# Performance work log

Hardware: AMD Instinct MI355X
Metric: run time of the kernel (lower is better)

## Reference

```python
import jax, jax.numpy as jnp
import numpy as np

B, H, W, C = 8, 64, 64, 512
C8, C2 = C // 8, C // 2  # f/g channels = 64, h channels = 256 (divisor = 2)


def _maxpool2x2(t):
    # [B, H, W, F] -> [B, H//2, W//2, F], valid 2x2 max pooling
    b, h, w, f = t.shape
    return t.reshape(b, h // 2, 2, w // 2, 2, f).max(axis=(2, 4))


def setup_inputs() -> dict:
    key = jax.random.key(0)
    kx, kf, kg, kh, ko, kgam = jax.random.split(key, 6)
    sf = lambda fan_in: (1.0 / np.sqrt(fan_in)).astype(np.float32)
    return {
        "x": jax.random.normal(kx, (B, H, W, C), dtype=jnp.float32),
        "wf": jax.random.normal(kf, (C, C8), dtype=jnp.float32) * sf(C),
        "wg": jax.random.normal(kg, (C, C8), dtype=jnp.float32) * sf(C),
        "wh": jax.random.normal(kh, (C, C2), dtype=jnp.float32) * sf(C),
        "wo": jax.random.normal(ko, (C2, C), dtype=jnp.float32) * sf(C2),
        "gamma": jax.random.normal(kgam, (1,), dtype=jnp.float32) * 0.1,
    }


def reference(x, wf, wg, wh, wo, gamma):
    b = x.shape[0]
    # 1x1 convs == channel matmuls
    f = _maxpool2x2(jnp.einsum("bhwc,cd->bhwd", x, wf)).reshape(b, -1, C8)  # [B, N/4, C/8]
    g = jnp.einsum("bhwc,cd->bhwd", x, wg).reshape(b, -1, C8)               # [B, N,   C/8]
    s = jnp.einsum("bqd,bkd->bqk", g, f)                                     # unscaled scores
    beta = jax.nn.softmax(s, axis=-1)
    h = _maxpool2x2(jnp.einsum("bhwc,cd->bhwd", x, wh)).reshape(b, -1, C2)  # [B, N/4, C/2]
    o = jnp.einsum("bqk,bkd->bqd", beta, h).reshape(b, H, W, C2)
    o = jnp.einsum("bhwd,dc->bhwc", o, wo)                                   # o_conv back to C
    return gamma * o + x
```

## Files before the change

### kernel.cpp

```cpp
#include <hip/hip_runtime.h>
#include <hip/hip_bf16.h>

#define NTOK 4096
#define NPOOL 1024

using short8 = __attribute__((ext_vector_type(8))) short;
using f32x4  = __attribute__((ext_vector_type(4))) float;

__device__ __forceinline__ unsigned short f2bf(float f) {
  __hip_bfloat16 h = __float2bfloat16(f);
  return __builtin_bit_cast(unsigned short, h);
}

__device__ __forceinline__ int pool_row(int bx, int m) {
  int pg = bx * 16 + (m >> 2);
  int corner = m & 3;
  int batch = pg >> 10;
  int pl = pg & 1023;
  int pi = pl >> 5, pj = pl & 31;
  return (batch << 12) + ((2 * pi + (corner >> 1)) << 6) + 2 * pj + (corner & 1);
}

__global__ __launch_bounds__(256) void pack_w(const float* __restrict__ wf,
                                              const float* __restrict__ wg,
                                              const float* __restrict__ wh,
                                              const float* __restrict__ wo,
                                              unsigned short* __restrict__ wcatT,
                                              unsigned short* __restrict__ woT) {
  int i = blockIdx.x * 256 + threadIdx.x;
  if (i < 384 * 512) {
    int n = i >> 9, k = i & 511;
    float v = (n < 64) ? wf[k * 64 + n]
            : (n < 128) ? wg[k * 64 + (n - 64)]
                        : wh[k * 256 + (n - 128)];
    wcatT[i] = f2bf(v);
  } else if (i < 384 * 512 + 512 * 256) {
    int j = i - 384 * 512;
    int n = j >> 8, k = j & 255;
    woT[j] = f2bf(wo[(size_t)k * 512 + n]);
  }
}

__global__ __launch_bounds__(256) void fgh_proj(const float* __restrict__ x,
                                                const unsigned short* __restrict__ wcatT,
                                                unsigned short* __restrict__ fB,
                                                unsigned short* __restrict__ gB,
                                                unsigned short* __restrict__ hT) {
  __shared__ unsigned short lds[17920];
  const int tid = threadIdx.x;
  const int bx = blockIdx.x;
  const int wave = tid >> 6, lane = tid & 63;
  const int col = lane & 15, rgrp = lane >> 4;

  f32x4 acc[4][6];
#pragma unroll
  for (int mt = 0; mt < 4; ++mt)
#pragma unroll
    for (int nt = 0; nt < 6; ++nt) acc[mt][nt] = (f32x4){0.f, 0.f, 0.f, 0.f};

  for (int kt = 0; kt < 16; ++kt) {
    __syncthreads();
#pragma unroll
    for (int r = 0; r < 2; ++r) {
      int idx = tid + r * 256;
      int m = idx >> 3, k4 = (idx & 7) << 2;
      float4 v = *(const float4*)(x + (size_t)pool_row(bx, m) * 512 + kt * 32 + k4);
      ushort4 o4;
      o4.x = f2bf(v.x); o4.y = f2bf(v.y); o4.z = f2bf(v.z); o4.w = f2bf(v.w);
      *(ushort4*)&lds[m * 40 + k4] = o4;
    }
#pragma unroll
    for (int r = 0; r < 6; ++r) {
      int idx = tid + r * 256;
      int n = idx >> 2, k8 = (idx & 3) << 3;
      *(uint4*)&lds[2560 + n * 40 + k8] =
          *(const uint4*)(wcatT + (size_t)n * 512 + kt * 32 + k8);
    }
    __syncthreads();

    short8 am[4];
#pragma unroll
    for (int mt = 0; mt < 4; ++mt)
      am[mt] = *(const short8*)&lds[(mt * 16 + col) * 40 + rgrp * 8];
#pragma unroll
    for (int nt = 0; nt < 6; ++nt) {
      short8 bn = *(const short8*)&lds[2560 + (wave * 96 + nt * 16 + col) * 40 + rgrp * 8];
#pragma unroll
      for (int mt = 0; mt < 4; ++mt)
        acc[mt][nt] = __builtin_amdgcn_mfma_f32_16x16x32_bf16(am[mt], bn, acc[mt][nt], 0, 0, 0);
    }
  }
  __syncthreads();

  unsigned short* gO = lds;
  unsigned short* fO = lds + 4608;
  unsigned short* hO = lds + 5760;
#pragma unroll
  for (int mt = 0; mt < 4; ++mt) {
#pragma unroll
    for (int nt = 0; nt < 6; ++nt) {
      int n = wave * 96 + nt * 16 + col;
      f32x4 a = acc[mt][nt];
      if (n < 64) {
        float mx = fmaxf(fmaxf(a[0], a[1]), fmaxf(a[2], a[3]));
        fO[(mt * 4 + rgrp) * 72 + n] = f2bf(mx);
      } else if (n < 128) {
#pragma unroll
        for (int reg = 0; reg < 4; ++reg)
          gO[(mt * 16 + rgrp * 4 + reg) * 72 + (n - 64)] = f2bf(a[reg]);
      } else {
        float mx = fmaxf(fmaxf(a[0], a[1]), fmaxf(a[2], a[3]));
        hO[(n - 128) * 24 + (mt * 4 + rgrp)] = f2bf(mx);
      }
    }
  }
  __syncthreads();

  const int b = bx >> 6, pkb = (bx & 63) * 16;
#pragma unroll
  for (int r = 0; r < 2; ++r) {
    int idx = tid + r * 256;
    int m = idx >> 3, d8 = (idx & 7) << 3;
    *(uint4*)(gB + (size_t)pool_row(bx, m) * 64 + d8) = *(const uint4*)&gO[m * 72 + d8];
  }
  if (tid < 128) {
    int pr = tid >> 3, d8 = (tid & 7) << 3;
    *(uint4*)(fB + (size_t)(bx * 16 + pr) * 64 + d8) = *(const uint4*)&fO[pr * 72 + d8];
  }
#pragma unroll
  for (int r = 0; r < 2; ++r) {
    int idx = tid + r * 256;
    int dv = idx >> 1, p8 = (idx & 1) << 3;
    *(uint4*)(hT + (((size_t)b * 256 + dv) << 10) + pkb + p8) = *(const uint4*)&hO[dv * 24 + p8];
  }
}

__global__ __launch_bounds__(256) void attn_mfma(const __hip_bfloat16* __restrict__ G,
                                                 const __hip_bfloat16* __restrict__ F,
                                                 const __hip_bfloat16* __restrict__ HT,
                                                 unsigned short* __restrict__ O) {
  __shared__ __hip_bfloat16 gS[64][72];
  __shared__ __hip_bfloat16 fS[64][72];
  __shared__ __hip_bfloat16 hS[256][72];
  __shared__ __hip_bfloat16 pS[64][72];

  const int tid = threadIdx.x;
  const int wave = tid >> 6, lane = tid & 63;
  const int col = lane & 15;
  const int rgrp = lane >> 4;
  const int b = blockIdx.x >> 6, qt = blockIdx.x & 63;

  const __hip_bfloat16* Gb = G + ((size_t)b * NTOK + qt * 64) * 64;
  const __hip_bfloat16* Fb = F + (size_t)b * NPOOL * 64;
  const __hip_bfloat16* Hb = HT + (size_t)b * 256 * NPOOL;

#pragma unroll
  for (int r = 0; r < 2; ++r) {
    int j = tid + r * 256;
    int q = j >> 3, d8 = (j & 7) << 3;
    *(uint4*)&gS[q][d8] = *(const uint4*)(Gb + (size_t)q * 64 + d8);
  }
  __syncthreads();

  short8 ag[2];
#pragma unroll
  for (int ks = 0; ks < 2; ++ks)
    ag[ks] = *(const short8*)&gS[wave * 16 + col][ks * 32 + rgrp * 8];

  f32x4 oacc[16];
#pragma unroll
  for (int t = 0; t < 16; ++t) oacc[t] = (f32x4){0.f, 0.f, 0.f, 0.f};
  float m_run[4], l_run[4];
#pragma unroll
  for (int r = 0; r < 4; ++r) { m_run[r] = -1e30f; l_run[r] = 0.f; }

  for (int kc = 0; kc < 16; ++kc) {
    __syncthreads();
#pragma unroll
    for (int r = 0; r < 2; ++r) {
      int j = tid + r * 256;
      int k = j >> 3, d8 = (j & 7) << 3;
      *(uint4*)&fS[k][d8] = *(const uint4*)(Fb + (size_t)(kc * 64 + k) * 64 + d8);
    }
#pragma unroll
    for (int r = 0; r < 8; ++r) {
      int j = tid + r * 256;
      int dv = j >> 3, k8 = (j & 7) << 3;
      *(uint4*)&hS[dv][k8] = *(const uint4*)(Hb + (size_t)dv * NPOOL + kc * 64 + k8);
    }
    __syncthreads();

    f32x4 s[4];
#pragma unroll
    for (int t = 0; t < 4; ++t) s[t] = (f32x4){0.f, 0.f, 0.f, 0.f};
#pragma unroll
    for (int ks = 0; ks < 2; ++ks) {
#pragma unroll
      for (int t = 0; t < 4; ++t) {
        short8 bf = *(const short8*)&fS[t * 16 + col][ks * 32 + rgrp * 8];
        s[t] = __builtin_amdgcn_mfma_f32_16x16x32_bf16(ag[ks], bf, s[t], 0, 0, 0);
      }
    }

    float cm[4];
#pragma unroll
    for (int r = 0; r < 4; ++r) {
      cm[r] = fmaxf(fmaxf(s[0][r], s[1][r]), fmaxf(s[2][r], s[3][r]));
#pragma unroll
      for (int msk = 1; msk < 16; msk <<= 1) cm[r] = fmaxf(cm[r], __shfl_xor(cm[r], msk));
    }
    float alpha[4], rs[4];
#pragma unroll
    for (int r = 0; r < 4; ++r) {
      float mn = fmaxf(m_run[r], cm[r]);
      alpha[r] = __expf(m_run[r] - mn);
      m_run[r] = mn;
      rs[r] = 0.f;
    }
    const int prow = wave * 16 + rgrp * 4;
#pragma unroll
    for (int t = 0; t < 4; ++t) {
#pragma unroll
      for (int r = 0; r < 4; ++r) {
        float p = __expf(s[t][r] - m_run[r]);
        rs[r] += p;
        pS[prow + r][t * 16 + col] = __float2bfloat16(p);
      }
    }
#pragma unroll
    for (int r = 0; r < 4; ++r) {
#pragma unroll
      for (int msk = 1; msk < 16; msk <<= 1) rs[r] += __shfl_xor(rs[r], msk);
      l_run[r] = alpha[r] * l_run[r] + rs[r];
    }

#pragma unroll
    for (int t = 0; t < 16; ++t) {
#pragma unroll
      for (int r = 0; r < 4; ++r) oacc[t][r] *= alpha[r];
    }

    short8 ap[2];
#pragma unroll
    for (int ks = 0; ks < 2; ++ks)
      ap[ks] = *(const short8*)&pS[wave * 16 + col][ks * 32 + rgrp * 8];
#pragma unroll
    for (int t = 0; t < 16; ++t) {
#pragma unroll
      for (int ks = 0; ks < 2; ++ks) {
        short8 bh = *(const short8*)&hS[t * 16 + col][ks * 32 + rgrp * 8];
        oacc[t] = __builtin_amdgcn_mfma_f32_16x16x32_bf16(ap[ks], bh, oacc[t], 0, 0, 0);
      }
    }
  }

  float inv[4];
#pragma unroll
  for (int r = 0; r < 4; ++r) inv[r] = 1.0f / l_run[r];
  __syncthreads();
  unsigned short* oS = (unsigned short*)&hS[0][0];
  const int qrow = wave * 16 + rgrp * 4;
#pragma unroll
  for (int t = 0; t < 16; ++t) {
#pragma unroll
    for (int r = 0; r < 4; ++r)
      oS[(qrow + r) * 264 + t * 16 + col] = f2bf(oacc[t][r] * inv[r]);
  }
  __syncthreads();
  unsigned short* Ob = O + ((size_t)b * NTOK + qt * 64) * 256;
#pragma unroll
  for (int r = 0; r < 8; ++r) {
    int idx = tid + r * 256;
    int q = idx >> 5, d8 = (idx & 31) << 3;
    *(uint4*)(Ob + (size_t)q * 256 + d8) = *(const uint4*)&oS[q * 264 + d8];
  }
}

__global__ __launch_bounds__(256) void gemm_out_mfma(const unsigned short* __restrict__ Obf,
                                                     const unsigned short* __restrict__ woT,
                                                     const float* __restrict__ Xres,
                                                     const float* __restrict__ gamma,
                                                     float* __restrict__ Out) {
  __shared__ unsigned short lds[23040];
  const int tid = threadIdx.x;
  const int bx = blockIdx.x;
  const int wave = tid >> 6, lane = tid & 63;
  const int col = lane & 15, rgrp = lane >> 4;

  f32x4 acc[4][8];
#pragma unroll
  for (int mt = 0; mt < 4; ++mt)
#pragma unroll
    for (int nt = 0; nt < 8; ++nt) acc[mt][nt] = (f32x4){0.f, 0.f, 0.f, 0.f};

  for (int kt = 0; kt < 8; ++kt) {
    __syncthreads();
    {
      int m = tid >> 2, k8 = (tid & 3) << 3;
      *(uint4*)&lds[m * 40 + k8] =
          *(const uint4*)(Obf + ((size_t)bx * 64 + m) * 256 + kt * 32 + k8);
    }
#pragma unroll
    for (int r = 0; r < 8; ++r) {
      int idx = tid + r * 256;
      int n = idx >> 2, k8 = (idx & 3) << 3;
      *(uint4*)&lds[2560 + n * 40 + k8] =
          *(const uint4*)(woT + (size_t)n * 256 + kt * 32 + k8);
    }
    __syncthreads();

    short8 am[4];
#pragma unroll
    for (int mt = 0; mt < 4; ++mt)
      am[mt] = *(const short8*)&lds[(mt * 16 + col) * 40 + rgrp * 8];
#pragma unroll
    for (int nt = 0; nt < 8; ++nt) {
      short8 bn = *(const short8*)&lds[2560 + (wave * 128 + nt * 16 + col) * 40 + rgrp * 8];
#pragma unroll
      for (int mt = 0; mt < 4; ++mt)
        acc[mt][nt] = __builtin_amdgcn_mfma_f32_16x16x32_bf16(am[mt], bn, acc[mt][nt], 0, 0, 0);
    }
  }

  float gm = gamma[0];
#pragma unroll
  for (int mt = 0; mt < 4; ++mt) {
#pragma unroll
    for (int nt = 0; nt < 8; ++nt) {
      int n = wave * 128 + nt * 16 + col;
#pragma unroll
      for (int reg = 0; reg < 4; ++reg) {
        size_t row = (size_t)bx * 64 + mt * 16 + rgrp * 4 + reg;
        size_t off = row * 512 + n;
        Out[off] = gm * acc[mt][nt][reg] + Xres[off];
      }
    }
  }
}

extern "C" void kernel_launch(void* const* d_in, const int* in_sizes, int n_in,
                              void* d_out, int out_size, void* d_ws, size_t ws_size,
                              hipStream_t stream) {
  (void)in_sizes; (void)n_in; (void)out_size; (void)ws_size;
  const float* x     = (const float*)d_in[0];
  const float* wf    = (const float*)d_in[1];
  const float* wg    = (const float*)d_in[2];
  const float* wh    = (const float*)d_in[3];
  const float* wo    = (const float*)d_in[4];
  const float* gamma = (const float*)d_in[5];
  float* out = (float*)d_out;

  unsigned short* ws = (unsigned short*)d_ws;
  unsigned short* oB    = ws;
  unsigned short* gB    = ws + 8388608;
  unsigned short* fB    = ws + 10485760;
  unsigned short* hT    = ws + 11010048;
  unsigned short* wcatT = ws + 13107200;
  unsigned short* woT   = ws + 13303808;

  dim3 blk(256);
  pack_w<<<1280, blk, 0, stream>>>(wf, wg, wh, wo, wcatT, woT);
  fgh_proj<<<512, blk, 0, stream>>>(x, wcatT, fB, gB, hT);
  attn_mfma<<<512, blk, 0, stream>>>((const __hip_bfloat16*)gB, (const __hip_bfloat16*)fB,
                                     (const __hip_bfloat16*)hT, oB);
  gemm_out_mfma<<<512, blk, 0, stream>>>(oB, woT, x, gamma, out);
}
```

Measured before the change: 262.0 us.

## Split attention across key halves and shrink tiles to double block counts

The attention kernel is split into two blocks per query tile, each covering half of the pooled keys and writing partial outputs with running max and sum. A new combine kernel merges the two halves. The projection kernel now uses 32-row tiles and the output GEMM splits the N dimension across a second grid axis, so each stage launches more blocks to fill the 256 CUs. The cost is an extra launch, extra workspace traffic for the partial outputs, and lower per-block reuse from the smaller tiles.

Measured after the change: 290.2 us. 1.11x slower.

```diff
diff --git a/kernel.cpp b/kernel.cpp
--- a/kernel.cpp
+++ b/kernel.cpp
@@ -4,16 +4,21 @@
 #define NTOK 4096
 #define NPOOL 1024
 
-using short8 = __attribute__((ext_vector_type(8))) short;
-using f32x4  = __attribute__((ext_vector_type(4))) float;
+using short8  = __attribute__((ext_vector_type(8))) short;
+using ushort8 = __attribute__((ext_vector_type(8))) unsigned short;
+using f32x4   = __attribute__((ext_vector_type(4))) float;
 
 __device__ __forceinline__ unsigned short f2bf(float f) {
   __hip_bfloat16 h = __float2bfloat16(f);
   return __builtin_bit_cast(unsigned short, h);
 }
-
-__device__ __forceinline__ int pool_row(int bx, int m) {
-  int pg = bx * 16 + (m >> 2);
+__device__ __forceinline__ float bf2f(unsigned short u) {
+  unsigned int t = ((unsigned int)u) << 16;
+  return __builtin_bit_cast(float, t);
+}
+
+__device__ __forceinline__ int pool_row8(int bx, int m) {
+  int pg = bx * 8 + (m >> 2);
   int corner = m & 3;
   int batch = pg >> 10;
   int pl = pg & 1023;
@@ -46,57 +51,55 @@
                                                 unsigned short* __restrict__ fB,
                                                 unsigned short* __restrict__ gB,
                                                 unsigned short* __restrict__ hT) {
-  __shared__ unsigned short lds[17920];
+  __shared__ unsigned short lds[16640];
   const int tid = threadIdx.x;
   const int bx = blockIdx.x;
   const int wave = tid >> 6, lane = tid & 63;
   const int col = lane & 15, rgrp = lane >> 4;
 
-  f32x4 acc[4][6];
-#pragma unroll
-  for (int mt = 0; mt < 4; ++mt)
+  const int mA = tid >> 3, k4A = (tid & 7) << 2;
+  const int rowA = pool_row8(bx, mA);
+  const int nW = tid >> 2, k8W = (tid & 3) << 3;
+
+  f32x4 acc[2][6];
+#pragma unroll
+  for (int mt = 0; mt < 2; ++mt)
 #pragma unroll
     for (int nt = 0; nt < 6; ++nt) acc[mt][nt] = (f32x4){0.f, 0.f, 0.f, 0.f};
 
   for (int kt = 0; kt < 16; ++kt) {
     __syncthreads();
-#pragma unroll
-    for (int r = 0; r < 2; ++r) {
-      int idx = tid + r * 256;
-      int m = idx >> 3, k4 = (idx & 7) << 2;
-      float4 v = *(const float4*)(x + (size_t)pool_row(bx, m) * 512 + kt * 32 + k4);
+    {
+      float4 v = *(const float4*)(x + (size_t)rowA * 512 + kt * 32 + k4A);
       ushort4 o4;
       o4.x = f2bf(v.x); o4.y = f2bf(v.y); o4.z = f2bf(v.z); o4.w = f2bf(v.w);
-      *(ushort4*)&lds[m * 40 + k4] = o4;
-    }
-#pragma unroll
-    for (int r = 0; r < 6; ++r) {
-      int idx = tid + r * 256;
-      int n = idx >> 2, k8 = (idx & 3) << 3;
-      *(uint4*)&lds[2560 + n * 40 + k8] =
-          *(const uint4*)(wcatT + (size_t)n * 512 + kt * 32 + k8);
-    }
-    __syncthreads();
-
-    short8 am[4];
-#pragma unroll
-    for (int mt = 0; mt < 4; ++mt)
+      *(ushort4*)&lds[mA * 40 + k4A] = o4;
+#pragma unroll
+      for (int r = 0; r < 6; ++r)
+        *(uint4*)&lds[1280 + (nW + r * 64) * 40 + k8W] =
+            *(const uint4*)(wcatT + (size_t)(nW + r * 64) * 512 + kt * 32 + k8W);
+    }
+    __syncthreads();
+
+    short8 am[2];
+#pragma unroll
+    for (int mt = 0; mt < 2; ++mt)
       am[mt] = *(const short8*)&lds[(mt * 16 + col) * 40 + rgrp * 8];
 #pragma unroll
     for (int nt = 0; nt < 6; ++nt) {
-      short8 bn = *(const short8*)&lds[2560 + (wave * 96 + nt * 16 + col) * 40 + rgrp * 8];
-#pragma unroll
-      for (int mt = 0; mt < 4; ++mt)
+      short8 bn = *(const short8*)&lds[1280 + (wave * 96 + nt * 16 + col) * 40 + rgrp * 8];
+#pragma unroll
+      for (int mt = 0; mt < 2; ++mt)
         acc[mt][nt] = __builtin_amdgcn_mfma_f32_16x16x32_bf16(am[mt], bn, acc[mt][nt], 0, 0, 0);
     }
   }
   __syncthreads();
 
   unsigned short* gO = lds;
-  unsigned short* fO = lds + 4608;
-  unsigned short* hO = lds + 5760;
-#pragma unroll
-  for (int mt = 0; mt < 4; ++mt) {
+  unsigned short* fO = lds + 2304;
+  unsigned short* hO = lds + 2880;
+#pragma unroll
+  for (int mt = 0; mt < 2; ++mt) {
 #pragma unroll
     for (int nt = 0; nt < 6; ++nt) {
       int n = wave * 96 + nt * 16 + col;
@@ -110,62 +113,55 @@
           gO[(mt * 16 + rgrp * 4 + reg) * 72 + (n - 64)] = f2bf(a[reg]);
       } else {
         float mx = fmaxf(fmaxf(a[0], a[1]), fmaxf(a[2], a[3]));
-        hO[(n - 128) * 24 + (mt * 4 + rgrp)] = f2bf(mx);
+        hO[(n - 128) * 16 + (mt * 4 + rgrp)] = f2bf(mx);
       }
     }
   }
   __syncthreads();
 
-  const int b = bx >> 6, pkb = (bx & 63) * 16;
-#pragma unroll
-  for (int r = 0; r < 2; ++r) {
-    int idx = tid + r * 256;
-    int m = idx >> 3, d8 = (idx & 7) << 3;
-    *(uint4*)(gB + (size_t)pool_row(bx, m) * 64 + d8) = *(const uint4*)&gO[m * 72 + d8];
-  }
-  if (tid < 128) {
+  const int b = bx >> 7, pkb = (bx & 127) * 8;
+  {
+    int m = tid >> 3, d8 = (tid & 7) << 3;
+    *(uint4*)(gB + (size_t)pool_row8(bx, m) * 64 + d8) = *(const uint4*)&gO[m * 72 + d8];
+  }
+  if (tid < 64) {
     int pr = tid >> 3, d8 = (tid & 7) << 3;
-    *(uint4*)(fB + (size_t)(bx * 16 + pr) * 64 + d8) = *(const uint4*)&fO[pr * 72 + d8];
-  }
-#pragma unroll
-  for (int r = 0; r < 2; ++r) {
-    int idx = tid + r * 256;
-    int dv = idx >> 1, p8 = (idx & 1) << 3;
-    *(uint4*)(hT + (((size_t)b * 256 + dv) << 10) + pkb + p8) = *(const uint4*)&hO[dv * 24 + p8];
-  }
-}
-
-__global__ __launch_bounds__(256) void attn_mfma(const __hip_bfloat16* __restrict__ G,
-                                                 const __hip_bfloat16* __restrict__ F,
-                                                 const __hip_bfloat16* __restrict__ HT,
-                                                 unsigned short* __restrict__ O) {
-  __shared__ __hip_bfloat16 gS[64][72];
-  __shared__ __hip_bfloat16 fS[64][72];
-  __shared__ __hip_bfloat16 hS[256][72];
-  __shared__ __hip_bfloat16 pS[64][72];
-
+    *(uint4*)(fB + (size_t)(bx * 8 + pr) * 64 + d8) = *(const uint4*)&fO[pr * 72 + d8];
+  }
+  {
+    int dv = tid;
+    *(uint4*)(hT + (((size_t)b * 256 + dv) << 10) + pkb) = *(const uint4*)&hO[dv * 16];
+  }
+}
+
+__global__ __launch_bounds__(256) void attn_split(const __hip_bfloat16* __restrict__ G,
+                                                  const __hip_bfloat16* __restrict__ F,
+                                                  const __hip_bfloat16* __restrict__ HT,
+                                                  unsigned short* __restrict__ Op,
+                                                  float* __restrict__ ML) {
+  __shared__ unsigned short lds[19712];
   const int tid = threadIdx.x;
   const int wave = tid >> 6, lane = tid & 63;
-  const int col = lane & 15;
-  const int rgrp = lane >> 4;
-  const int b = blockIdx.x >> 6, qt = blockIdx.x & 63;
+  const int col = lane & 15, rgrp = lane >> 4;
+  const int bx = blockIdx.x;
+  const int split = bx & 1, qt = (bx >> 1) & 63, b = bx >> 7;
 
   const __hip_bfloat16* Gb = G + ((size_t)b * NTOK + qt * 64) * 64;
-  const __hip_bfloat16* Fb = F + (size_t)b * NPOOL * 64;
-  const __hip_bfloat16* Hb = HT + (size_t)b * 256 * NPOOL;
+  const __hip_bfloat16* Fb = F + ((size_t)b * NPOOL + split * 512) * 64;
+  const __hip_bfloat16* Hb = HT + (size_t)b * 256 * NPOOL + split * 512;
 
 #pragma unroll
   for (int r = 0; r < 2; ++r) {
     int j = tid + r * 256;
     int q = j >> 3, d8 = (j & 7) << 3;
-    *(uint4*)&gS[q][d8] = *(const uint4*)(Gb + (size_t)q * 64 + d8);
+    *(uint4*)&lds[q * 72 + d8] = *(const uint4*)(Gb + (size_t)q * 64 + d8);
   }
   __syncthreads();
 
   short8 ag[2];
 #pragma unroll
   for (int ks = 0; ks < 2; ++ks)
-    ag[ks] = *(const short8*)&gS[wave * 16 + col][ks * 32 + rgrp * 8];
+    ag[ks] = *(const short8*)&lds[(wave * 16 + col) * 72 + ks * 32 + rgrp * 8];
 
   f32x4 oacc[16];
 #pragma unroll
@@ -174,30 +170,29 @@
 #pragma unroll
   for (int r = 0; r < 4; ++r) { m_run[r] = -1e30f; l_run[r] = 0.f; }
 
+  const int fk = tid >> 3, fd8 = (tid & 7) << 3;
+
   for (int kc = 0; kc < 16; ++kc) {
     __syncthreads();
-#pragma unroll
-    for (int r = 0; r < 2; ++r) {
+    *(uint4*)&lds[4608 + fk * 72 + fd8] =
+        *(const uint4*)(Fb + (size_t)(kc * 32 + fk) * 64 + fd8);
+#pragma unroll
+    for (int r = 0; r < 4; ++r) {
       int j = tid + r * 256;
-      int k = j >> 3, d8 = (j & 7) << 3;
-      *(uint4*)&fS[k][d8] = *(const uint4*)(Fb + (size_t)(kc * 64 + k) * 64 + d8);
-    }
-#pragma unroll
-    for (int r = 0; r < 8; ++r) {
-      int j = tid + r * 256;
-      int dv = j >> 3, k8 = (j & 7) << 3;
-      *(uint4*)&hS[dv][k8] = *(const uint4*)(Hb + (size_t)dv * NPOOL + kc * 64 + k8);
-    }
-    __syncthreads();
-
-    f32x4 s[4];
-#pragma unroll
-    for (int t = 0; t < 4; ++t) s[t] = (f32x4){0.f, 0.f, 0.f, 0.f};
+      int dv = j >> 2, k8 = (j & 3) << 3;
+      *(uint4*)&lds[6912 + dv * 40 + k8] =
+          *(const uint4*)(Hb + (size_t)dv * NPOOL + kc * 32 + k8);
+    }
+    __syncthreads();
+
+    f32x4 s[2];
+#pragma unroll
+    for (int t = 0; t < 2; ++t) s[t] = (f32x4){0.f, 0.f, 0.f, 0.f};
 #pragma unroll
     for (int ks = 0; ks < 2; ++ks) {
 #pragma unroll
-      for (int t = 0; t < 4; ++t) {
-        short8 bf = *(const short8*)&fS[t * 16 + col][ks * 32 + rgrp * 8];
+      for (int t = 0; t < 2; ++t) {
+        short8 bf = *(const short8*)&lds[4608 + (t * 16 + col) * 72 + ks * 32 + rgrp * 8];
         s[t] = __builtin_amdgcn_mfma_f32_16x16x32_bf16(ag[ks], bf, s[t], 0, 0, 0);
       }
     }
@@ -205,7 +200,7 @@
     float cm[4];
 #pragma unroll
     for (int r = 0; r < 4; ++r) {
-      cm[r] = fmaxf(fmaxf(s[0][r], s[1][r]), fmaxf(s[2][r], s[3][r]));
+      cm[r] = fmaxf(s[0][r], s[1][r]);
 #pragma unroll
       for (int msk = 1; msk < 16; msk <<= 1) cm[r] = fmaxf(cm[r], __shfl_xor(cm[r], msk));
     }
@@ -219,12 +214,12 @@
     }
     const int prow = wave * 16 + rgrp * 4;
 #pragma unroll
-    for (int t = 0; t < 4; ++t) {
+    for (int t = 0; t < 2; ++t) {
 #pragma unroll
       for (int r = 0; r < 4; ++r) {
         float p = __expf(s[t][r] - m_run[r]);
         rs[r] += p;
-        pS[prow + r][t * 16 + col] = __float2bfloat16(p);
+        lds[17152 + (prow + r) * 40 + t * 16 + col] = f2bf(p);
       }
     }
 #pragma unroll
@@ -240,17 +235,11 @@
       for (int r = 0; r < 4; ++r) oacc[t][r] *= alpha[r];
     }
 
-    short8 ap[2];
-#pragma unroll
-    for (int ks = 0; ks < 2; ++ks)
-      ap[ks] = *(const short8*)&pS[wave * 16 + col][ks * 32 + rgrp * 8];
+    short8 ap = *(const short8*)&lds[17152 + (wave * 16 + col) * 40 + rgrp * 8];
 #pragma unroll
     for (int t = 0; t < 16; ++t) {
-#pragma unroll
-      for (int ks = 0; ks < 2; ++ks) {
-        short8 bh = *(const short8*)&hS[t * 16 + col][ks * 32 + rgrp * 8];
-        oacc[t] = __builtin_amdgcn_mfma_f32_16x16x32_bf16(ap[ks], bh, oacc[t], 0, 0, 0);
-      }
+      short8 bh = *(const short8*)&lds[6912 + (t * 16 + col) * 40 + rgrp * 8];
+      oacc[t] = __builtin_amdgcn_mfma_f32_16x16x32_bf16(ap, bh, oacc[t], 0, 0, 0);
     }
   }
 
@@ -258,22 +247,49 @@
 #pragma unroll
   for (int r = 0; r < 4; ++r) inv[r] = 1.0f / l_run[r];
   __syncthreads();
-  unsigned short* oS = (unsigned short*)&hS[0][0];
   const int qrow = wave * 16 + rgrp * 4;
 #pragma unroll
   for (int t = 0; t < 16; ++t) {
 #pragma unroll
     for (int r = 0; r < 4; ++r)
-      oS[(qrow + r) * 264 + t * 16 + col] = f2bf(oacc[t][r] * inv[r]);
-  }
-  __syncthreads();
-  unsigned short* Ob = O + ((size_t)b * NTOK + qt * 64) * 256;
+      lds[(qrow + r) * 264 + t * 16 + col] = f2bf(oacc[t][r] * inv[r]);
+  }
+  if (col == 0) {
+    float2* mlp = (float2*)ML;
+    const size_t rowg = (size_t)b * NTOK + qt * 64 + qrow;
+#pragma unroll
+    for (int r = 0; r < 4; ++r)
+      mlp[(size_t)split * 32768 + rowg + r] = make_float2(m_run[r], l_run[r]);
+  }
+  __syncthreads();
+  unsigned short* Ob = Op + (size_t)split * 8388608 + ((size_t)b * NTOK + qt * 64) * 256;
 #pragma unroll
   for (int r = 0; r < 8; ++r) {
     int idx = tid + r * 256;
     int q = idx >> 5, d8 = (idx & 31) << 3;
-    *(uint4*)(Ob + (size_t)q * 256 + d8) = *(const uint4*)&oS[q * 264 + d8];
-  }
+    *(uint4*)(Ob + (size_t)q * 256 + d8) = *(const uint4*)&lds[q * 264 + d8];
+  }
+}
+
+__global__ __launch_bounds__(256) void combine_k(unsigned short* __restrict__ Op,
+                                                 const float* __restrict__ ML) {
+  int idx = blockIdx.x * 256 + threadIdx.x;
+  int row = idx >> 5, d8 = (idx & 31) << 3;
+  const float2* mlp = (const float2*)ML;
+  float2 a = mlp[row], bml = mlp[32768 + row];
+  float M = fmaxf(a.x, bml.x);
+  float w0 = __expf(a.x - M) * a.y;
+  float w1 = __expf(bml.x - M) * bml.y;
+  float inv = 1.0f / (w0 + w1);
+  float c0 = w0 * inv, c1 = w1 * inv;
+  size_t off = (size_t)row * 256 + d8;
+  ushort8 u0 = *(const ushort8*)(Op + off);
+  ushort8 u1 = *(const ushort8*)(Op + 8388608 + off);
+  ushort8 o;
+#pragma unroll
+  for (int i = 0; i < 8; ++i)
+    o[i] = f2bf(c0 * bf2f(u0[i]) + c1 * bf2f(u1[i]));
+  *(ushort8*)(Op + off) = o;
 }
 
 __global__ __launch_bounds__(256) void gemm_out_mfma(const unsigned short* __restrict__ Obf,
@@ -281,31 +297,30 @@
                                                      const float* __restrict__ Xres,
                                                      const float* __restrict__ gamma,
                                                      float* __restrict__ Out) {
-  __shared__ unsigned short lds[23040];
+  __shared__ unsigned short lds[12800];
   const int tid = threadIdx.x;
-  const int bx = blockIdx.x;
+  const int bx = blockIdx.x, by = blockIdx.y;
   const int wave = tid >> 6, lane = tid & 63;
   const int col = lane & 15, rgrp = lane >> 4;
 
-  f32x4 acc[4][8];
+  const int mA = tid >> 2, k8 = (tid & 3) << 3;
+
+  f32x4 acc[4][4];
 #pragma unroll
   for (int mt = 0; mt < 4; ++mt)
 #pragma unroll
-    for (int nt = 0; nt < 8; ++nt) acc[mt][nt] = (f32x4){0.f, 0.f, 0.f, 0.f};
+    for (int nt = 0; nt < 4; ++nt) acc[mt][nt] = (f32x4){0.f, 0.f, 0.f, 0.f};
 
   for (int kt = 0; kt < 8; ++kt) {
     __syncthreads();
-    {
-      int m = tid >> 2, k8 = (tid & 3) << 3;
-      *(uint4*)&lds[m * 40 + k8] =
-          *(const uint4*)(Obf + ((size_t)bx * 64 + m) * 256 + kt * 32 + k8);
-    }
-#pragma unroll
-    for (int r = 0; r < 8; ++r) {
+    *(uint4*)&lds[mA * 40 + k8] =
+        *(const uint4*)(Obf + ((size_t)bx * 64 + mA) * 256 + kt * 32 + k8);
+#pragma unroll
+    for (int r = 0; r < 4; ++r) {
       int idx = tid + r * 256;
-      int n = idx >> 2, k8 = (idx & 3) << 3;
-      *(uint4*)&lds[2560 + n * 40 + k8] =
-          *(const uint4*)(woT + (size_t)n * 256 + kt * 32 + k8);
+      int n = idx >> 2, k8w = (idx & 3) << 3;
+      *(uint4*)&lds[2560 + n * 40 + k8w] =
+          *(const uint4*)(woT + (size_t)(by * 256 + n) * 256 + kt * 32 + k8w);
     }
     __syncthreads();
 
@@ -314,8 +329,8 @@
     for (int mt = 0; mt < 4; ++mt)
       am[mt] = *(const short8*)&lds[(mt * 16 + col) * 40 + rgrp * 8];
 #pragma unroll
-    for (int nt = 0; nt < 8; ++nt) {
-      short8 bn = *(const short8*)&lds[2560 + (wave * 128 + nt * 16 + col) * 40 + rgrp * 8];
+    for (int nt = 0; nt < 4; ++nt) {
+      short8 bn = *(const short8*)&lds[2560 + (wave * 64 + nt * 16 + col) * 40 + rgrp * 8];
 #pragma unroll
       for (int mt = 0; mt < 4; ++mt)
         acc[mt][nt] = __builtin_amdgcn_mfma_f32_16x16x32_bf16(am[mt], bn, acc[mt][nt], 0, 0, 0);
@@ -326,8 +341,8 @@
 #pragma unroll
   for (int mt = 0; mt < 4; ++mt) {
 #pragma unroll
-    for (int nt = 0; nt < 8; ++nt) {
-      int n = wave * 128 + nt * 16 + col;
+    for (int nt = 0; nt < 4; ++nt) {
+      int n = by * 256 + wave * 64 + nt * 16 + col;
 #pragma unroll
       for (int reg = 0; reg < 4; ++reg) {
         size_t row = (size_t)bx * 64 + mt * 16 + rgrp * 4 + reg;
@@ -351,17 +366,19 @@
   float* out = (float*)d_out;
 
   unsigned short* ws = (unsigned short*)d_ws;
-  unsigned short* oB    = ws;
-  unsigned short* gB    = ws + 8388608;
-  unsigned short* fB    = ws + 10485760;
-  unsigned short* hT    = ws + 11010048;
-  unsigned short* wcatT = ws + 13107200;
-  unsigned short* woT   = ws + 13303808;
+  unsigned short* gB    = ws;
+  unsigned short* fB    = ws + 2097152;
+  unsigned short* hT    = ws + 2621440;
+  unsigned short* wcatT = ws + 4718592;
+  unsigned short* woT   = ws + 4915200;
+  unsigned short* Op    = ws + 5046272;
+  float*          ML    = (float*)(ws + 21823488);
 
   dim3 blk(256);
   pack_w<<<1280, blk, 0, stream>>>(wf, wg, wh, wo, wcatT, woT);
-  fgh_proj<<<512, blk, 0, stream>>>(x, wcatT, fB, gB, hT);
-  attn_mfma<<<512, blk, 0, stream>>>((const __hip_bfloat16*)gB, (const __hip_bfloat16*)fB,
-                                     (const __hip_bfloat16*)hT, oB);
-  gemm_out_mfma<<<512, blk, 0, stream>>>(oB, woT, x, gamma, out);
-}
+  fgh_proj<<<1024, blk, 0, stream>>>(x, wcatT, fB, gB, hT);
+  attn_split<<<1024, blk, 0, stream>>>((const __hip_bfloat16*)gB, (const __hip_bfloat16*)fB,
+                                       (const __hip_bfloat16*)hT, Op, ML);
+  combine_k<<<4096, blk, 0, stream>>>(Op, ML);
+  gemm_out_mfma<<<dim3(512, 2), blk, 0, stream>>>(Op, woT, x, gamma, out);
+}
```
